# Optimization experiments

Measured on AMD Instinct MI355X. Metric: run time of the kernel, lower is better.

Reference implementation:

```python
import jax, jax.numpy as jnp
import numpy as np

B, T, IN, H, OUT = 256, 512, 128, 1024, 9  # batch, seq_len, input_size, hidden_dim, output_size(=9 coords)


def setup_inputs() -> dict:
    key = jax.random.key(0)
    ks = jax.random.split(key, 10)
    rn = lambda k, sh: jax.random.normal(k, sh, dtype=jnp.float32) * 0.05
    return {
        "x": rn(ks[0], (B, T, IN)),
        "W_ih": rn(ks[1], (4 * H, IN + OUT)),   # LSTMCell input weights (input_size + 9)
        "b_ih": rn(ks[2], (4 * H,)),
        "W_hh": rn(ks[3], (4 * H, H)),
        "b_hh": rn(ks[4], (4 * H,)),
        "W_h2h": rn(ks[5], (H, H)),
        "b_h2h": rn(ks[6], (H,)),
        "W_h2o": rn(ks[7], (OUT, H)),
        "b_h2o": rn(ks[8], (OUT,)),
        "lengths": jax.random.randint(ks[9], (B,), 1, T + 1).astype(jnp.int32),
    }


def reference(x, W_ih, b_ih, W_hh, b_hh, W_h2h, b_h2h, W_h2o, b_h2o, lengths):
    # Faithful to SimpleCharRNN.forward with use_corrector_flag=False (default):
    # per timestep: concat(x_t, prev_output) -> LSTMCell -> h2h -> h2o,
    # and NOTE the h2h output replaces h as the recurrent hidden state.
    batch = x.shape[0]
    hid = W_hh.shape[1]
    out_dim = W_h2o.shape[0]

    def step(carry, xt):
        h, c, out_prev = carry
        inp = jnp.concatenate([xt, out_prev], axis=-1)           # [B, IN+9]
        gates = inp @ W_ih.T + b_ih + h @ W_hh.T + b_hh          # [B, 4H]
        i, f, g, o = jnp.split(gates, 4, axis=-1)                # torch LSTMCell gate order
        i = jax.nn.sigmoid(i)
        f = jax.nn.sigmoid(f)
        g = jnp.tanh(g)
        o = jax.nn.sigmoid(o)
        c_new = f * c + i * g
        h_cell = o * jnp.tanh(c_new)
        h_new = h_cell @ W_h2h.T + b_h2h                         # h <- h2h(h)
        out_new = h_new @ W_h2o.T + b_h2o                        # output_i = h2o(h)
        return (h_new, c_new, out_new), out_new

    h0 = jnp.zeros((batch, hid), x.dtype)
    c0 = jnp.zeros((batch, hid), x.dtype)
    o0 = jnp.zeros((batch, out_dim), x.dtype)
    _, outs = jax.lax.scan(step, (h0, c0, o0), jnp.swapaxes(x, 0, 1))  # outs: [T, B, 9]
    answer = jnp.swapaxes(outs, 0, 1)                            # [B, T, 9]
    return answer, lengths
```

## Files before the change

### kernel.cpp

```cpp
#include <hip/hip_runtime.h>
#include <math.h>

#define TB 256
#define TT 512
#define TIN 128
#define TH 1024
#define TOUT 9
#define KD 1152

typedef _Float16 half8 __attribute__((ext_vector_type(8)));
typedef float f32x4 __attribute__((ext_vector_type(4)));

#define OB_WHF   0ull
#define SB_WHF   (128ull*2*36*64*8*2)
#define OB_WCB   (OB_WHF + SB_WHF)
#define SB_WCB   (9ull*1024*4)
#define OB_BCB   (OB_WCB + SB_WCB)
#define SB_BCB   64ull
#define OB_B0    (OB_BCB + SB_BCB)
#define SB_B0    (4096ull*4)
#define OB_BC    (OB_B0 + SB_B0)
#define SB_BC    (4096ull*4)
#define OB_H0    (OB_BC + SB_BC)
#define SB_H     (256ull*1024*2)
#define OB_H1    (OB_H0 + SB_H)
#define OB_GC    (OB_H1 + SB_H)
#define OB_END   (OB_GC + 8192ull)

__device__ __forceinline__ size_t frag_addr(int col, int k) {
  int q = col >> 10, hcol = col & 1023;
  int wcg = hcol >> 3, jj = hcol & 7;
  int c = (q << 3) | jj;
  int nt = c >> 4, n = c & 15;
  int kc = k >> 5, ls = (k >> 3) & 3, je = k & 7;
  return ((((size_t)wcg * 2 + nt) * 36 + kc) * 64 + ((ls << 4) | n)) * 8 + je;
}

__device__ __forceinline__ void st_h16_agent(_Float16* p, uint4 v) {
  union { uint4 q; unsigned long long u[2]; } c; c.q = v;
  __hip_atomic_store((unsigned long long*)p,     c.u[0], __ATOMIC_RELAXED, __HIP_MEMORY_SCOPE_AGENT);
  __hip_atomic_store((unsigned long long*)p + 1, c.u[1], __ATOMIC_RELAXED, __HIP_MEMORY_SCOPE_AGENT);
}


__global__ __launch_bounds__(256) void k_combo(const float* __restrict__ W_h2o,
                                               const float* __restrict__ W_h2h,
                                               const float* __restrict__ b_h2h,
                                               const float* __restrict__ b_h2o,
                                               float* __restrict__ Wcombo,
                                               float* __restrict__ bcombo) {
  int gid = blockIdx.x * 256 + threadIdx.x;
  if (gid < 9 * 1024) {
    int r = gid >> 10, m = gid & 1023;
    float s = 0.f;
    for (int j = 0; j < 1024; ++j) s += W_h2o[r * 1024 + j] * W_h2h[j * 1024 + m];
    Wcombo[gid] = s;
  }
  if (gid < 9) {
    float s = b_h2o[gid];
    for (int j = 0; j < 1024; ++j) s += W_h2o[gid * 1024 + j] * b_h2h[j];
    bcombo[gid] = s;
  }
}

__global__ __launch_bounds__(256) void k_wblk(const float* __restrict__ W_hh,
                                              const float* __restrict__ W_ih,
                                              const float* __restrict__ W_h2o,
                                              const float* __restrict__ W_h2h,
                                              _Float16* __restrict__ Whf) {
  __shared__ float As2[16][68];
  __shared__ float Bs[16][68];
  __shared__ float Wio_s[64][12];
  __shared__ float Bo[9][16];
  const int tid = threadIdx.x;
  const int bm = (blockIdx.x & 15) * 64;
  const int bc = (blockIdx.x >> 4) * 64;
  const int tx = tid & 15, ty = tid >> 4;
  const int cl = tid >> 2, kq4 = tid & 3;

  for (int i = tid; i < 64 * 9; i += 256) {
    int row = i / 9, r = i % 9;
    Wio_s[row][r] = W_ih[(size_t)(bc + row) * 137 + 128 + r];
  }

  float acc[4][4];
#pragma unroll
  for (int i = 0; i < 4; ++i)
#pragma unroll
    for (int j = 0; j < 4; ++j) acc[i][j] = 0.f;

  for (int k0 = 0; k0 < 1024; k0 += 16) {
    __syncthreads();
    if (tid < 144) { int r = tid >> 4, kk = tid & 15; Bo[r][kk] = W_h2o[(size_t)r * 1024 + k0 + kk]; }
    { int kk = tid >> 4, q = tid & 15;
      float4 v = *(const float4*)(W_h2h + (size_t)(k0 + kk) * 1024 + bm + q * 4);
      *(float4*)&Bs[kk][q * 4] = v; }
    float4 av = *(const float4*)(W_hh + (size_t)(bc + cl) * 1024 + k0 + kq4 * 4);
    __syncthreads();
    {
      float c0 = 0.f, c1 = 0.f, c2 = 0.f, c3 = 0.f;
#pragma unroll
      for (int r = 0; r < 9; ++r) {
        float wio = Wio_s[cl][r];
        c0 += wio * Bo[r][kq4 * 4 + 0];
        c1 += wio * Bo[r][kq4 * 4 + 1];
        c2 += wio * Bo[r][kq4 * 4 + 2];
        c3 += wio * Bo[r][kq4 * 4 + 3];
      }
      As2[kq4 * 4 + 0][cl] = av.x + c0;
      As2[kq4 * 4 + 1][cl] = av.y + c1;
      As2[kq4 * 4 + 2][cl] = av.z + c2;
      As2[kq4 * 4 + 3][cl] = av.w + c3;
    }
    __syncthreads();
#pragma unroll
    for (int kk = 0; kk < 16; ++kk) {
      float4 a = *(const float4*)&As2[kk][ty * 4];
      float4 bv = *(const float4*)&Bs[kk][tx * 4];
      acc[0][0] += a.x * bv.x; acc[0][1] += a.x * bv.y; acc[0][2] += a.x * bv.z; acc[0][3] += a.x * bv.w;
      acc[1][0] += a.y * bv.x; acc[1][1] += a.y * bv.y; acc[1][2] += a.y * bv.z; acc[1][3] += a.y * bv.w;
      acc[2][0] += a.z * bv.x; acc[2][1] += a.z * bv.y; acc[2][2] += a.z * bv.z; acc[2][3] += a.z * bv.w;
      acc[3][0] += a.w * bv.x; acc[3][1] += a.w * bv.y; acc[3][2] += a.w * bv.z; acc[3][3] += a.w * bv.w;
    }
  }
#pragma unroll
  for (int i = 0; i < 4; ++i)
#pragma unroll
    for (int j = 0; j < 4; ++j) {
      int col = bc + ty * 4 + i;
      int m = bm + tx * 4 + j;
      Whf[frag_addr(col, 128 + m)] = (_Float16)acc[i][j];
    }
}

__global__ __launch_bounds__(256) void k_bias(const float* __restrict__ b_ih,
                                              const float* __restrict__ b_hh,
                                              const float* __restrict__ W_hh,
                                              const float* __restrict__ W_ih,
                                              const float* __restrict__ b_h2h,
                                              const float* __restrict__ bcombo,
                                              float* __restrict__ b0,
                                              float* __restrict__ bconst) {
  int col = blockIdx.x * 256 + threadIdx.x;
  float base = b_ih[col] + b_hh[col];
  b0[col] = base;
  float s = 0.f;
  for (int j = 0; j < 1024; ++j) s += W_hh[(size_t)col * 1024 + j] * b_h2h[j];
#pragma unroll
  for (int r = 0; r < 9; ++r) s += W_ih[(size_t)col * 137 + 128 + r] * bcombo[r];
  bconst[col] = base + s;
}

__global__ __launch_bounds__(256) void k_fillx(const float* __restrict__ W_ih,
                                               _Float16* __restrict__ Whf) {
  int gid = blockIdx.x * 256 + threadIdx.x;
  int col = gid >> 7, k = gid & 127;
  Whf[frag_addr(col, k)] = (_Float16)W_ih[(size_t)col * 137 + k];
}

__global__ void k_len(const int* __restrict__ len, float* __restrict__ dout) {
  int i = threadIdx.x;
  if (i < TB) dout[(size_t)TB * TT * TOUT + i] = (float)len[i];
}


__device__ __forceinline__ float sigm(float v) { return 1.f / (1.f + __expf(-v)); }
__device__ __forceinline__ float tanh_f(float v) {
  float e2 = __expf(2.f * v);
  return (e2 - 1.f) / (e2 + 1.f);
}

#define KEEP18(a) asm volatile("" :: "v"(a[0]), "v"(a[1]), "v"(a[2]), "v"(a[3]), \
  "v"(a[4]), "v"(a[5]), "v"(a[6]), "v"(a[7]), "v"(a[8]), "v"(a[9]), "v"(a[10]), \
  "v"(a[11]), "v"(a[12]), "v"(a[13]), "v"(a[14]), "v"(a[15]), "v"(a[16]), "v"(a[17]))

__global__ __launch_bounds__(512, 2) void k_main(const float* __restrict__ x,
                                                 const _Float16* __restrict__ Whf,
                                                 const float* __restrict__ Wc,
                                                 const float* __restrict__ b0,
                                                 const float* __restrict__ bcf,
                                                 const float* __restrict__ bcombo,
                                                 _Float16* __restrict__ hA,
                                                 _Float16* __restrict__ hB,
                                                 unsigned* __restrict__ gs,
                                                 float* __restrict__ dout) {
  __shared__ _Float16 Wl[2 * 36 * 64 * 8];
  __shared__ float gbuf[2][128][36];
  __shared__ float Wc_s[9][1024];
  __shared__ _Float16 htmp[128][8];
  __shared__ float bias_s[2][32];
  __shared__ float bco_s[12];
  __shared__ int sAbort;

  const int bx = blockIdx.x;
  const int half_id = bx >> 7;
  const int wcg = bx & 127;
  const int B0 = half_id * 128;
  const int myb = B0 + wcg;
  const int grp = wcg >> 4;
  const int tid = threadIdx.x;
  const int lane = tid & 63;
  const int wv = tid >> 6;
  const int mp = wv & 3, kh = wv >> 2;

  const size_t CH = (size_t)TB * 8;

  unsigned* hbase = gs + half_id * 1024;
  unsigned* gcnt_grp = hbase + grp * 32;
  unsigned* gcnt_root = hbase + 8 * 32;
  unsigned* gabort = gs + 1984;

  {
    const uint4* src = (const uint4*)(Whf + (size_t)wcg * (2 * 36 * 64 * 8));
    uint4* dst = (uint4*)Wl;
    for (int i = tid; i < 2 * 36 * 64 * 8 / 8; i += 512) dst[i] = src[i];
  }
  {
    const float4* src = (const float4*)Wc;
    float4* dst = (float4*)&Wc_s[0][0];
    for (int i = tid; i < 9 * 1024 / 4; i += 512) dst[i] = src[i];
  }
  if (tid == 0) sAbort = 0;
  if (tid < 9) bco_s[tid] = bcombo[tid];
  if (tid < 32) {
    int g = (tid >> 3) * 1024 + wcg * 8 + (tid & 7);
    bias_s[0][tid] = b0[g];
    bias_s[1][tid] = bcf[g];
  }
  float cs0 = 0.f, cs1 = 0.f;
  __syncthreads();

  const _Float16* ha = hA;
  _Float16* hn = hB;

  const int bA0 = B0 + mp * 32 + (lane & 15);
  const int bA1 = bA0 + 16;
  const int ko = (lane >> 4) * 8;
  const int chb = lane >> 4;
  const _Float16* wlb = Wl + (size_t)lane * 8 + (size_t)(kh * 18) * 512;
  unsigned myLead = 0;

  for (int t = 0; t < TT; ++t) {
    const _Float16* hb0 = ha + (size_t)chb * CH + (size_t)bA0 * 8;
    const _Float16* hb1 = ha + (size_t)chb * CH + (size_t)bA1 * 8;
    half8 a0[18], a1[18];
    if (kh == 0) {
      const float* x0 = x + ((size_t)bA0 * TT + t) * TIN;
      const float* x1 = x + ((size_t)bA1 * TT + t) * TIN;
      float4 xv0[8], xv1[8];
#pragma unroll
      for (int i = 0; i < 4; ++i) {
        xv0[2 * i]     = *(const float4*)(x0 + i * 32 + ko);
        xv0[2 * i + 1] = *(const float4*)(x0 + i * 32 + ko + 4);
        xv1[2 * i]     = *(const float4*)(x1 + i * 32 + ko);
        xv1[2 * i + 1] = *(const float4*)(x1 + i * 32 + ko + 4);
      }
#pragma unroll
      for (int lc = 4; lc < 18; ++lc) {
        a0[lc] = *(const half8*)(hb0 + (size_t)(4 * lc - 16) * CH);
        a1[lc] = *(const half8*)(hb1 + (size_t)(4 * lc - 16) * CH);
      }
#pragma unroll
      for (int i = 0; i < 4; ++i) {
        half8 v0, v1;
        v0[0] = (_Float16)xv0[2 * i].x; v0[1] = (_Float16)xv0[2 * i].y;
        v0[2] = (_Float16)xv0[2 * i].z; v0[3] = (_Float16)xv0[2 * i].w;
        v0[4] = (_Float16)xv0[2 * i + 1].x; v0[5] = (_Float16)xv0[2 * i + 1].y;
        v0[6] = (_Float16)xv0[2 * i + 1].z; v0[7] = (_Float16)xv0[2 * i + 1].w;
        v1[0] = (_Float16)xv1[2 * i].x; v1[1] = (_Float16)xv1[2 * i].y;
        v1[2] = (_Float16)xv1[2 * i].z; v1[3] = (_Float16)xv1[2 * i].w;
        v1[4] = (_Float16)xv1[2 * i + 1].x; v1[5] = (_Float16)xv1[2 * i + 1].y;
        v1[6] = (_Float16)xv1[2 * i + 1].z; v1[7] = (_Float16)xv1[2 * i + 1].w;
        a0[i] = v0; a1[i] = v1;
      }
    } else {
#pragma unroll
      for (int lc = 0; lc < 18; ++lc) {
        a0[lc] = *(const half8*)(hb0 + (size_t)(4 * lc + 56) * CH);
        a1[lc] = *(const half8*)(hb1 + (size_t)(4 * lc + 56) * CH);
      }
    }
    KEEP18(a0);
    KEEP18(a1);
    __builtin_amdgcn_sched_barrier(0);

    f32x4 acc00 = {0.f, 0.f, 0.f, 0.f};
    f32x4 acc01 = {0.f, 0.f, 0.f, 0.f};
    f32x4 acc10 = {0.f, 0.f, 0.f, 0.f};
    f32x4 acc11 = {0.f, 0.f, 0.f, 0.f};
#pragma unroll
    for (int lc = 0; lc < 18; ++lc) {
      half8 bf0 = *(const half8*)(wlb + (size_t)lc * 512);
      half8 bf1 = *(const half8*)(wlb + (size_t)(36 + lc) * 512);
      acc00 = __builtin_amdgcn_mfma_f32_16x16x32_f16(a0[lc], bf0, acc00, 0, 0, 0);
      acc01 = __builtin_amdgcn_mfma_f32_16x16x32_f16(a0[lc], bf1, acc01, 0, 0, 0);
      acc10 = __builtin_amdgcn_mfma_f32_16x16x32_f16(a1[lc], bf0, acc10, 0, 0, 0);
      acc11 = __builtin_amdgcn_mfma_f32_16x16x32_f16(a1[lc], bf1, acc11, 0, 0, 0);
    }
    {
      int rb0 = mp * 32 + (lane >> 4) * 4;
      int rb1 = rb0 + 16;
      int cc = lane & 15;
#pragma unroll
      for (int r = 0; r < 4; ++r) {
        gbuf[kh][rb0 + r][cc] = acc00[r];
        gbuf[kh][rb0 + r][16 + cc] = acc01[r];
        gbuf[kh][rb1 + r][cc] = acc10[r];
        gbuf[kh][rb1 + r][16 + cc] = acc11[r];
      }
    }
    __syncthreads();

    {
      const int fb = tid >> 3, fj = tid & 7;
      const float* bs = bias_s[(t > 0) ? 1 : 0];
      float vi = gbuf[0][fb][fj]      + gbuf[1][fb][fj]      + bs[fj];
      float vf = gbuf[0][fb][8 + fj]  + gbuf[1][fb][8 + fj]  + bs[8 + fj];
      float vg = gbuf[0][fb][16 + fj] + gbuf[1][fb][16 + fj] + bs[16 + fj];
      float vo = gbuf[0][fb][24 + fj] + gbuf[1][fb][24 + fj] + bs[24 + fj];
      float ig = sigm(vi), fg = sigm(vf), gg = tanh_f(vg), og = sigm(vo);
      float cn = fg * cs0 + ig * gg;
      cs0 = cn;
      htmp[fb][fj] = (_Float16)(og * tanh_f(cn));

      const int fb2 = fb + 64;
      float vi2 = gbuf[0][fb2][fj]      + gbuf[1][fb2][fj]      + bs[fj];
      float vf2 = gbuf[0][fb2][8 + fj]  + gbuf[1][fb2][8 + fj]  + bs[8 + fj];
      float vg2 = gbuf[0][fb2][16 + fj] + gbuf[1][fb2][16 + fj] + bs[16 + fj];
      float vo2 = gbuf[0][fb2][24 + fj] + gbuf[1][fb2][24 + fj] + bs[24 + fj];
      float ig2 = sigm(vi2), fg2 = sigm(vf2), gg2 = tanh_f(vg2), og2 = sigm(vo2);
      float cn2 = fg2 * cs1 + ig2 * gg2;
      cs1 = cn2;
      htmp[fb2][fj] = (_Float16)(og2 * tanh_f(cn2));
    }
    __syncthreads();

    if (tid < 128) {
      uint4 hv = *(const uint4*)&htmp[tid][0];
      st_h16_agent(hn + (size_t)wcg * CH + (size_t)(B0 + tid) * 8, hv);
    }
    __threadfence_block();
    __syncthreads();

    if (tid == 0) {
      unsigned old = __hip_atomic_fetch_add(gcnt_grp, 1u, __ATOMIC_RELAXED, __HIP_MEMORY_SCOPE_AGENT);
      myLead = (old == (unsigned)(t + 1) * 16u - 1u);
      if (myLead)
        __hip_atomic_fetch_add(gcnt_root, 1u, __ATOMIC_RELAXED, __HIP_MEMORY_SCOPE_AGENT);
    }

    if (t > 0) {
      const _Float16* hxb = ha + (size_t)myb * 8;
#pragma unroll
      for (int p = 0; p < 2; ++p) {
        int ch = 2 * lane + p;
        half8 hv = *(const half8*)(hxb + (size_t)ch * CH);
        const float* wr = &Wc_s[wv][ch * 8];
        float s = 0.f;
#pragma unroll
        for (int j = 0; j < 8; ++j) s += (float)hv[j] * wr[j];
        if (p == 0) {
#pragma unroll
          for (int off = 32; off > 0; off >>= 1) s += __shfl_down(s, off, 64);
          if (lane == 0) dout[((size_t)myb * TT + (t - 1)) * TOUT + wv] = s + bco_s[wv];
        } else {
          float s2 = s;
#pragma unroll
          for (int off = 32; off > 0; off >>= 1) s2 += __shfl_down(s2, off, 64);
          if (lane == 0) dout[((size_t)myb * TT + (t - 1)) * TOUT + wv] += s2;
        }
      }
      if (wv == 0) {
        const float* wr8 = &Wc_s[8][0];
        float s = 0.f;
#pragma unroll
        for (int p = 0; p < 2; ++p) {
          int ch = 2 * lane + p;
          half8 hv = *(const half8*)(hxb + (size_t)ch * CH);
#pragma unroll
          for (int j = 0; j < 8; ++j) s += (float)hv[j] * wr8[ch * 8 + j];
        }
#pragma unroll
        for (int off = 32; off > 0; off >>= 1) s += __shfl_down(s, off, 64);
        if (lane == 0) dout[((size_t)myb * TT + (t - 1)) * TOUT + 8] = s + bco_s[8];
      }
    }

    if (tid == 0) {
      bool ab = false;
      unsigned guard = 0;
      const unsigned tgt = (unsigned)(t + 1) * 8u;
      while (__hip_atomic_load(gcnt_root, __ATOMIC_RELAXED, __HIP_MEMORY_SCOPE_AGENT) < tgt) {
        __builtin_amdgcn_s_sleep(1);
        if (((++guard) & 255u) == 0u &&
            __hip_atomic_load(gabort, __ATOMIC_RELAXED, __HIP_MEMORY_SCOPE_AGENT) != 0u) { ab = true; break; }
        if (guard > 200000u) {
          __hip_atomic_store(gabort, 1u, __ATOMIC_RELAXED, __HIP_MEMORY_SCOPE_AGENT);
          ab = true; break;
        }
      }
      if (ab) {
        sAbort = 1;
      } else {
        (void)__hip_atomic_load(gcnt_root, __ATOMIC_ACQUIRE, __HIP_MEMORY_SCOPE_AGENT);
      }
    }
    __syncthreads();
    if (sAbort) return;

    const _Float16* tp = ha; ha = hn; hn = (_Float16*)tp;
  }

  {
    const _Float16* hxb = ha + (size_t)myb * 8;
    {
      float s = 0.f;
#pragma unroll
      for (int p = 0; p < 2; ++p) {
        int ch = 2 * lane + p;
        half8 hv = *(const half8*)(hxb + (size_t)ch * CH);
        const float* wr = &Wc_s[wv][ch * 8];
#pragma unroll
        for (int j = 0; j < 8; ++j) s += (float)hv[j] * wr[j];
      }
#pragma unroll
      for (int off = 32; off > 0; off >>= 1) s += __shfl_down(s, off, 64);
      if (lane == 0) dout[((size_t)myb * TT + (TT - 1)) * TOUT + wv] = s + bco_s[wv];
    }
    if (wv == 0) {
      const float* wr8 = &Wc_s[8][0];
      float s = 0.f;
#pragma unroll
      for (int p = 0; p < 2; ++p) {
        int ch = 2 * lane + p;
        half8 hv = *(const half8*)(hxb + (size_t)ch * CH);
#pragma unroll
        for (int j = 0; j < 8; ++j) s += (float)hv[j] * wr8[ch * 8 + j];
      }
#pragma unroll
      for (int off = 32; off > 0; off >>= 1) s += __shfl_down(s, off, 64);
      if (lane == 0) dout[((size_t)myb * TT + (TT - 1)) * TOUT + 8] = s + bco_s[8];
    }
  }
}


extern "C" void kernel_launch(void* const* d_in, const int* in_sizes, int n_in,
                              void* d_out, int out_size, void* d_ws, size_t ws_size,
                              hipStream_t stream) {
  if (ws_size < OB_END) return;

  const float* x     = (const float*)d_in[0];
  const float* W_ih  = (const float*)d_in[1];
  const float* b_ih  = (const float*)d_in[2];
  const float* W_hh  = (const float*)d_in[3];
  const float* b_hh  = (const float*)d_in[4];
  const float* W_h2h = (const float*)d_in[5];
  const float* b_h2h = (const float*)d_in[6];
  const float* W_h2o = (const float*)d_in[7];
  const float* b_h2o = (const float*)d_in[8];
  const int*   lens  = (const int*)d_in[9];

  char* ws = (char*)d_ws;
  float* dout    = (float*)d_out;
  _Float16* Whf  = (_Float16*)(ws + OB_WHF);
  float* Wcombo  = (float*)(ws + OB_WCB);
  float* bcombo  = (float*)(ws + OB_BCB);
  float* b0      = (float*)(ws + OB_B0);
  float* bconst  = (float*)(ws + OB_BC);
  _Float16* h0   = (_Float16*)(ws + OB_H0);
  _Float16* h1   = (_Float16*)(ws + OB_H1);
  unsigned* gs   = (unsigned*)(ws + OB_GC);

  hipMemsetAsync((void*)(ws + OB_H0), 0, OB_END - OB_H0, stream);

  k_combo<<<36, 256, 0, stream>>>(W_h2o, W_h2h, b_h2h, b_h2o, Wcombo, bcombo);
  k_wblk<<<1024, 256, 0, stream>>>(W_hh, W_ih, W_h2o, W_h2h, Whf);
  k_bias<<<16, 256, 0, stream>>>(b_ih, b_hh, W_hh, W_ih, b_h2h, bcombo, b0, bconst);
  k_fillx<<<2048, 256, 0, stream>>>(W_ih, Whf);
  k_len<<<1, 256, 0, stream>>>(lens, dout);

  k_main<<<256, 512, 0, stream>>>(x, Whf, Wcombo, b0, bconst, bcombo, h0, h1, gs, dout);
}
```

Before: 5.460 ms.

## Precompute next step's x-projection during barrier wait and store h directly

The x_t input contribution (the first 4 K-chunks of the MFMA) for step t+1 is now computed before the grid-wide spin wait, so it overlaps the synchronization latency instead of sitting on the critical path after the barrier. The htmp shared staging buffer and its __syncthreads are removed. Each thread instead writes its h value straight to global with 2-byte agent-scope atomic stores. The two-pass output reduction is merged into a single shuffle reduction. The trade is many small scattered global stores in place of 16-byte ones, plus the accumulators being live across the wait.

```diff
diff --git a/kernel.cpp b/kernel.cpp
--- a/kernel.cpp
+++ b/kernel.cpp
@@ -36,10 +36,9 @@
   return ((((size_t)wcg * 2 + nt) * 36 + kc) * 64 + ((ls << 4) | n)) * 8 + je;
 }
 
-__device__ __forceinline__ void st_h16_agent(_Float16* p, uint4 v) {
-  union { uint4 q; unsigned long long u[2]; } c; c.q = v;
-  __hip_atomic_store((unsigned long long*)p,     c.u[0], __ATOMIC_RELAXED, __HIP_MEMORY_SCOPE_AGENT);
-  __hip_atomic_store((unsigned long long*)p + 1, c.u[1], __ATOMIC_RELAXED, __HIP_MEMORY_SCOPE_AGENT);
+__device__ __forceinline__ void st_h2_agent(_Float16* p, _Float16 v) {
+  union { _Float16 h; unsigned short u; } c; c.h = v;
+  __hip_atomic_store((unsigned short*)p, c.u, __ATOMIC_RELAXED, __HIP_MEMORY_SCOPE_AGENT);
 }
 
 
@@ -170,6 +169,9 @@
   return (e2 - 1.f) / (e2 + 1.f);
 }
 
+#define KEEP14(a) asm volatile("" :: "v"(a[0]), "v"(a[1]), "v"(a[2]), "v"(a[3]), \
+  "v"(a[4]), "v"(a[5]), "v"(a[6]), "v"(a[7]), "v"(a[8]), "v"(a[9]), "v"(a[10]), \
+  "v"(a[11]), "v"(a[12]), "v"(a[13]))
 #define KEEP18(a) asm volatile("" :: "v"(a[0]), "v"(a[1]), "v"(a[2]), "v"(a[3]), \
   "v"(a[4]), "v"(a[5]), "v"(a[6]), "v"(a[7]), "v"(a[8]), "v"(a[9]), "v"(a[10]), \
   "v"(a[11]), "v"(a[12]), "v"(a[13]), "v"(a[14]), "v"(a[15]), "v"(a[16]), "v"(a[17]))
@@ -187,7 +189,6 @@
   __shared__ _Float16 Wl[2 * 36 * 64 * 8];
   __shared__ float gbuf[2][128][36];
   __shared__ float Wc_s[9][1024];
-  __shared__ _Float16 htmp[128][8];
   __shared__ float bias_s[2][32];
   __shared__ float bco_s[12];
   __shared__ int sAbort;
@@ -240,62 +241,76 @@
   const _Float16* wlb = Wl + (size_t)lane * 8 + (size_t)(kh * 18) * 512;
   unsigned myLead = 0;
 
+  f32x4 acc00 = {0.f, 0.f, 0.f, 0.f};
+  f32x4 acc01 = {0.f, 0.f, 0.f, 0.f};
+  f32x4 acc10 = {0.f, 0.f, 0.f, 0.f};
+  f32x4 acc11 = {0.f, 0.f, 0.f, 0.f};
+
+#define XPART(tt) do { \
+    const float* x0_ = x + ((size_t)bA0 * TT + (tt)) * TIN; \
+    const float* x1_ = x + ((size_t)bA1 * TT + (tt)) * TIN; \
+    _Pragma("unroll") \
+    for (int i_ = 0; i_ < 4; ++i_) { \
+      float4 p0 = *(const float4*)(x0_ + i_ * 32 + ko); \
+      float4 p1 = *(const float4*)(x0_ + i_ * 32 + ko + 4); \
+      float4 q0 = *(const float4*)(x1_ + i_ * 32 + ko); \
+      float4 q1 = *(const float4*)(x1_ + i_ * 32 + ko + 4); \
+      half8 v0_, v1_; \
+      v0_[0] = (_Float16)p0.x; v0_[1] = (_Float16)p0.y; v0_[2] = (_Float16)p0.z; v0_[3] = (_Float16)p0.w; \
+      v0_[4] = (_Float16)p1.x; v0_[5] = (_Float16)p1.y; v0_[6] = (_Float16)p1.z; v0_[7] = (_Float16)p1.w; \
+      v1_[0] = (_Float16)q0.x; v1_[1] = (_Float16)q0.y; v1_[2] = (_Float16)q0.z; v1_[3] = (_Float16)q0.w; \
+      v1_[4] = (_Float16)q1.x; v1_[5] = (_Float16)q1.y; v1_[6] = (_Float16)q1.z; v1_[7] = (_Float16)q1.w; \
+      half8 bf0_ = *(const half8*)(wlb + (size_t)i_ * 512); \
+      half8 bf1_ = *(const half8*)(wlb + (size_t)(36 + i_) * 512); \
+      acc00 = __builtin_amdgcn_mfma_f32_16x16x32_f16(v0_, bf0_, acc00, 0, 0, 0); \
+      acc01 = __builtin_amdgcn_mfma_f32_16x16x32_f16(v0_, bf1_, acc01, 0, 0, 0); \
+      acc10 = __builtin_amdgcn_mfma_f32_16x16x32_f16(v1_, bf0_, acc10, 0, 0, 0); \
+      acc11 = __builtin_amdgcn_mfma_f32_16x16x32_f16(v1_, bf1_, acc11, 0, 0, 0); \
+    } \
+  } while (0)
+
+  if (kh == 0) XPART(0);
+
   for (int t = 0; t < TT; ++t) {
     const _Float16* hb0 = ha + (size_t)chb * CH + (size_t)bA0 * 8;
     const _Float16* hb1 = ha + (size_t)chb * CH + (size_t)bA1 * 8;
-    half8 a0[18], a1[18];
     if (kh == 0) {
-      const float* x0 = x + ((size_t)bA0 * TT + t) * TIN;
-      const float* x1 = x + ((size_t)bA1 * TT + t) * TIN;
-      float4 xv0[8], xv1[8];
-#pragma unroll
-      for (int i = 0; i < 4; ++i) {
-        xv0[2 * i]     = *(const float4*)(x0 + i * 32 + ko);
-        xv0[2 * i + 1] = *(const float4*)(x0 + i * 32 + ko + 4);
-        xv1[2 * i]     = *(const float4*)(x1 + i * 32 + ko);
-        xv1[2 * i + 1] = *(const float4*)(x1 + i * 32 + ko + 4);
-      }
-#pragma unroll
-      for (int lc = 4; lc < 18; ++lc) {
-        a0[lc] = *(const half8*)(hb0 + (size_t)(4 * lc - 16) * CH);
-        a1[lc] = *(const half8*)(hb1 + (size_t)(4 * lc - 16) * CH);
-      }
-#pragma unroll
-      for (int i = 0; i < 4; ++i) {
-        half8 v0, v1;
-        v0[0] = (_Float16)xv0[2 * i].x; v0[1] = (_Float16)xv0[2 * i].y;
-        v0[2] = (_Float16)xv0[2 * i].z; v0[3] = (_Float16)xv0[2 * i].w;
-        v0[4] = (_Float16)xv0[2 * i + 1].x; v0[5] = (_Float16)xv0[2 * i + 1].y;
-        v0[6] = (_Float16)xv0[2 * i + 1].z; v0[7] = (_Float16)xv0[2 * i + 1].w;
-        v1[0] = (_Float16)xv1[2 * i].x; v1[1] = (_Float16)xv1[2 * i].y;
-        v1[2] = (_Float16)xv1[2 * i].z; v1[3] = (_Float16)xv1[2 * i].w;
-        v1[4] = (_Float16)xv1[2 * i + 1].x; v1[5] = (_Float16)xv1[2 * i + 1].y;
-        v1[6] = (_Float16)xv1[2 * i + 1].z; v1[7] = (_Float16)xv1[2 * i + 1].w;
-        a0[i] = v0; a1[i] = v1;
+      half8 a0[14], a1[14];
+#pragma unroll
+      for (int i = 0; i < 14; ++i) {
+        a0[i] = *(const half8*)(hb0 + (size_t)(4 * (4 + i) - 16) * CH);
+        a1[i] = *(const half8*)(hb1 + (size_t)(4 * (4 + i) - 16) * CH);
+      }
+      KEEP14(a0); KEEP14(a1);
+      __builtin_amdgcn_sched_barrier(0);
+#pragma unroll
+      for (int i = 0; i < 14; ++i) {
+        const int lc = 4 + i;
+        half8 bf0 = *(const half8*)(wlb + (size_t)lc * 512);
+        half8 bf1 = *(const half8*)(wlb + (size_t)(36 + lc) * 512);
+        acc00 = __builtin_amdgcn_mfma_f32_16x16x32_f16(a0[i], bf0, acc00, 0, 0, 0);
+        acc01 = __builtin_amdgcn_mfma_f32_16x16x32_f16(a0[i], bf1, acc01, 0, 0, 0);
+        acc10 = __builtin_amdgcn_mfma_f32_16x16x32_f16(a1[i], bf0, acc10, 0, 0, 0);
+        acc11 = __builtin_amdgcn_mfma_f32_16x16x32_f16(a1[i], bf1, acc11, 0, 0, 0);
       }
     } else {
-#pragma unroll
-      for (int lc = 0; lc < 18; ++lc) {
-        a0[lc] = *(const half8*)(hb0 + (size_t)(4 * lc + 56) * CH);
-        a1[lc] = *(const half8*)(hb1 + (size_t)(4 * lc + 56) * CH);
-      }
-    }
-    KEEP18(a0);
-    KEEP18(a1);
-    __builtin_amdgcn_sched_barrier(0);
-
-    f32x4 acc00 = {0.f, 0.f, 0.f, 0.f};
-    f32x4 acc01 = {0.f, 0.f, 0.f, 0.f};
-    f32x4 acc10 = {0.f, 0.f, 0.f, 0.f};
-    f32x4 acc11 = {0.f, 0.f, 0.f, 0.f};
-#pragma unroll
-    for (int lc = 0; lc < 18; ++lc) {
-      half8 bf0 = *(const half8*)(wlb + (size_t)lc * 512);
-      half8 bf1 = *(const half8*)(wlb + (size_t)(36 + lc) * 512);
-      acc00 = __builtin_amdgcn_mfma_f32_16x16x32_f16(a0[lc], bf0, acc00, 0, 0, 0);
-      acc01 = __builtin_amdgcn_mfma_f32_16x16x32_f16(a0[lc], bf1, acc01, 0, 0, 0);
-      acc10 = __builtin_amdgcn_mfma_f32_16x16x32_f16(a1[lc], bf0, acc10, 0, 0, 0);
-      acc11 = __builtin_amdgcn_mfma_f32_16x16x32_f16(a1[lc], bf1, acc11, 0, 0, 0);
+      half8 a0[18], a1[18];
+#pragma unroll
+      for (int i = 0; i < 18; ++i) {
+        a0[i] = *(const half8*)(hb0 + (size_t)(4 * i + 56) * CH);
+        a1[i] = *(const half8*)(hb1 + (size_t)(4 * i + 56) * CH);
+      }
+      KEEP18(a0); KEEP18(a1);
+      __builtin_amdgcn_sched_barrier(0);
+#pragma unroll
+      for (int i = 0; i < 18; ++i) {
+        half8 bf0 = *(const half8*)(wlb + (size_t)i * 512);
+        half8 bf1 = *(const half8*)(wlb + (size_t)(36 + i) * 512);
+        acc00 = __builtin_amdgcn_mfma_f32_16x16x32_f16(a0[i], bf0, acc00, 0, 0, 0);
+        acc01 = __builtin_amdgcn_mfma_f32_16x16x32_f16(a0[i], bf1, acc01, 0, 0, 0);
+        acc10 = __builtin_amdgcn_mfma_f32_16x16x32_f16(a1[i], bf0, acc10, 0, 0, 0);
+        acc11 = __builtin_amdgcn_mfma_f32_16x16x32_f16(a1[i], bf1, acc11, 0, 0, 0);
+      }
     }
     {
       int rb0 = mp * 32 + (lane >> 4) * 4;
@@ -321,7 +336,8 @@
       float ig = sigm(vi), fg = sigm(vf), gg = tanh_f(vg), og = sigm(vo);
       float cn = fg * cs0 + ig * gg;
       cs0 = cn;
-      htmp[fb][fj] = (_Float16)(og * tanh_f(cn));
+      st_h2_agent(hn + (size_t)wcg * CH + (size_t)(B0 + fb) * 8 + fj,
+                  (_Float16)(og * tanh_f(cn)));
 
       const int fb2 = fb + 64;
       float vi2 = gbuf[0][fb2][fj]      + gbuf[1][fb2][fj]      + bs[fj];
@@ -331,13 +347,8 @@
       float ig2 = sigm(vi2), fg2 = sigm(vf2), gg2 = tanh_f(vg2), og2 = sigm(vo2);
       float cn2 = fg2 * cs1 + ig2 * gg2;
       cs1 = cn2;
-      htmp[fb2][fj] = (_Float16)(og2 * tanh_f(cn2));
-    }
-    __syncthreads();
-
-    if (tid < 128) {
-      uint4 hv = *(const uint4*)&htmp[tid][0];
-      st_h16_agent(hn + (size_t)wcg * CH + (size_t)(B0 + tid) * 8, hv);
+      st_h2_agent(hn + (size_t)wcg * CH + (size_t)(B0 + fb2) * 8 + fj,
+                  (_Float16)(og2 * tanh_f(cn2)));
     }
     __threadfence_block();
     __syncthreads();
@@ -351,24 +362,19 @@
 
     if (t > 0) {
       const _Float16* hxb = ha + (size_t)myb * 8;
-#pragma unroll
-      for (int p = 0; p < 2; ++p) {
-        int ch = 2 * lane + p;
-        half8 hv = *(const half8*)(hxb + (size_t)ch * CH);
-        const float* wr = &Wc_s[wv][ch * 8];
+      {
         float s = 0.f;
 #pragma unroll
-        for (int j = 0; j < 8; ++j) s += (float)hv[j] * wr[j];
-        if (p == 0) {
-#pragma unroll
-          for (int off = 32; off > 0; off >>= 1) s += __shfl_down(s, off, 64);
-          if (lane == 0) dout[((size_t)myb * TT + (t - 1)) * TOUT + wv] = s + bco_s[wv];
-        } else {
-          float s2 = s;
-#pragma unroll
-          for (int off = 32; off > 0; off >>= 1) s2 += __shfl_down(s2, off, 64);
-          if (lane == 0) dout[((size_t)myb * TT + (t - 1)) * TOUT + wv] += s2;
+        for (int p = 0; p < 2; ++p) {
+          int ch = 2 * lane + p;
+          half8 hv = *(const half8*)(hxb + (size_t)ch * CH);
+          const float* wr = &Wc_s[wv][ch * 8];
+#pragma unroll
+          for (int j = 0; j < 8; ++j) s += (float)hv[j] * wr[j];
         }
+#pragma unroll
+        for (int off = 32; off > 0; off >>= 1) s += __shfl_down(s, off, 64);
+        if (lane == 0) dout[((size_t)myb * TT + (t - 1)) * TOUT + wv] = s + bco_s[wv];
       }
       if (wv == 0) {
         const float* wr8 = &Wc_s[8][0];
@@ -385,6 +391,12 @@
         if (lane == 0) dout[((size_t)myb * TT + (t - 1)) * TOUT + 8] = s + bco_s[8];
       }
     }
+
+    acc00 = (f32x4){0.f, 0.f, 0.f, 0.f};
+    acc01 = (f32x4){0.f, 0.f, 0.f, 0.f};
+    acc10 = (f32x4){0.f, 0.f, 0.f, 0.f};
+    acc11 = (f32x4){0.f, 0.f, 0.f, 0.f};
+    if (kh == 0 && t + 1 < TT) XPART(t + 1);
 
     if (tid == 0) {
       bool ab = false;
```

After: 5.049 ms. 1.08x faster.
